# Optimization experiments

Measured on AMD Instinct MI355X. Metric: run time of the kernel, lower is better.

## Reference

```python
import jax, jax.numpy as jnp
import numpy as np

B, N, FIN, FOUT = 16, 128, 128, 256   # batch, atoms(=max_atom), in_features, out_features
EOUT, BIN, BOUT, CI, L1 = 64, 14, 64, 64, 256


def _rnn_dir(x, wih, whh, bih, bhh):
    # x: [B, T, I]; torch nn.RNN step: h = tanh(x @ Wih^T + bih + h @ Whh^T + bhh)
    h0 = jnp.zeros((x.shape[0], whh.shape[0]), x.dtype)
    def step(h, xt):
        h = jnp.tanh(xt @ wih.T + bih + h @ whh.T + bhh)
        return h, h
    _, ys = jax.lax.scan(step, h0, jnp.swapaxes(x, 0, 1))
    return jnp.swapaxes(ys, 0, 1)  # [B, T, H]


def _bi_rnn(x, wih_f, whh_f, bih_f, bhh_f, wih_b, whh_b, bih_b, bhh_b):
    fwd = _rnn_dir(x, wih_f, whh_f, bih_f, bhh_f)
    bwd = _rnn_dir(x[:, ::-1, :], wih_b, whh_b, bih_b, bhh_b)[:, ::-1, :]
    return jnp.concatenate([fwd, bwd], axis=-1)  # [B, T, 2H]


def setup_inputs() -> dict:
    key = jax.random.key(0)
    ks = jax.random.split(key, 24)
    g = lambda i, shape, s=0.05: (jax.random.normal(ks[i], shape, jnp.float32) * s)
    return {
        "x": g(0, (B, N, FIN), 1.0),
        "adj": jax.random.randint(ks[1], (B, N, N), 0, 2).astype(jnp.int32),
        "w_edge": g(2, (B, N, N, BIN), 1.0),
        "W": g(3, (FIN, FOUT)),
        "a": g(4, (2 * FOUT, EOUT)),
        "wfc_w": g(5, (BIN, BOUT)), "wfc_b": g(6, (BOUT,)),
        "fc_w": g(7, (EOUT + BOUT, 1)), "fc_b": g(8, (1,)),
        "fcc_w": g(9, (FOUT, 1)), "fcc_b": g(10, (1,)),
        "wih_f": g(11, (CI, N)), "whh_f": g(12, (CI, CI)), "bih_f": g(13, (CI,)), "bhh_f": g(14, (CI,)),
        "wih_b": g(15, (CI, N)), "whh_b": g(16, (CI, CI)), "bih_b": g(17, (CI,)), "bhh_b": g(18, (CI,)),
        "fco_w": g(19, (2 * CI + FOUT, L1)), "fco_b": g(20, (L1,)),
    }


def reference(x, adj, w_edge, W, a, wfc_w, wfc_b, fc_w, fc_b, fcc_w, fcc_b,
              wih_f, whh_f, bih_f, bhh_f, wih_b, whh_b, bih_b, bhh_b, fco_w, fco_b):
    h = x @ W  # [B, N, FOUT]
    # faithful reproduction of the repeat/cat(dim=1)/view trick
    t1 = jnp.tile(h, (1, 1, N)).reshape(B, N * N, FOUT)  # row i*N+j = h_i
    t2 = jnp.tile(h, (1, N, 1))                          # row i*N+j = h_j
    atom_trans = jnp.concatenate([t1, t2], axis=1).reshape(B, N, N, 2 * FOUT)
    e = atom_trans @ a                                   # [B, N, N, EOUT]
    wproj = w_edge @ wfc_w + wfc_b                       # [B, N, N, BOUT]
    e = jax.nn.leaky_relu(jnp.concatenate([e, wproj], axis=3))
    e = (e @ fc_w + fc_b)[..., 0]                        # [B, N, N]
    att = jax.nn.softmax(jnp.where(adj > 0, e, jnp.float32(-9e15)), axis=2)
    # dropout is identity in eval mode
    at_in = att[..., None] * h[:, :, None, :]            # [B, N, N, FOUT], h_i broadcast over j
    hn = jax.nn.leaky_relu((at_in @ fcc_w + fcc_b)[..., 0])  # [B, N, N]
    hn = jax.nn.leaky_relu(_bi_rnn(hn, wih_f, whh_f, bih_f, bhh_f, wih_b, whh_b, bih_b, bhh_b))
    h1 = jnp.einsum('bij,bjf->bif', att, h)              # [B, N, FOUT]
    out = jnp.concatenate([hn, h1], axis=2) @ fco_w + fco_b  # [B, N, L1]
    return jax.nn.elu(out)
```

## Files before the change

kernel.cpp:

```cpp
#include <hip/hip_runtime.h>
#include <hip/hip_bf16.h>

#define DEV static __device__ __forceinline__

constexpr int B=16, N=128, FIN=128, FOUT=256, EOUT=64, BINW=14, BOUT=64, CI=64, L1=256;

constexpr int O_H   = 0;
constexpr int O_S   = O_H  + B*N*FOUT;
constexpr int O_SU  = O_S  + B*N;
constexpr int O_SV  = O_SU + B*N;
constexpr int O_ATT = O_SV + B*N;
constexpr int O_ZF  = O_ATT+ B*N*N;
constexpr int O_ZB  = O_ZF + B*N*CI;
constexpr int O_RF  = O_ZB + B*N*CI;
constexpr int O_RB  = O_RF + B*N*CI;
constexpr int O_H1  = O_RB + B*N*CI;

DEV float bf16_to_f32(unsigned short u){
  unsigned int x = ((unsigned int)u) << 16; float f;
  __builtin_memcpy(&f, &x, 4); return f;
}
DEV void bf2x(unsigned int u, float& lo, float& hi){
  unsigned int a = u << 16, b = u & 0xFFFF0000u;
  __builtin_memcpy(&lo, &a, 4); __builtin_memcpy(&hi, &b, 4);
}
DEV float lrelu(float x){ return x > 0.f ? x : 0.01f * x; }
DEV float bcastf(float v, int lane){
  return __builtin_bit_cast(float, __builtin_amdgcn_readlane(__builtin_bit_cast(int, v), lane));
}
DEV float ldf(const void* p, int i, int m){
  return m ? bf16_to_f32(((const unsigned short*)p)[i]) : ((const float*)p)[i];
}
DEV int blk_mode(const void* x, int nt, int tid){
  const unsigned short* u = (const unsigned short*)x;
  int e = (u[tid & 255] >> 7) & 0xFF;
  int cnt = __syncthreads_count(e >= 100 && e <= 140);
  return cnt * 4 >= nt * 3;
}

__global__ __launch_bounds__(256, 2) void k_h_pq(const void* __restrict__ xr,
                                                 const void* __restrict__ Wp,
                                                 const void* __restrict__ Ap,
                                                 const void* __restrict__ fccwp,
                                                 const void* __restrict__ fcwp,
                                                 float* __restrict__ ws){
  int blk = blockIdx.x, tid = threadIdx.x;
  int b = blk >> 5, i0 = (blk & 31) * 4;
  __shared__ __align__(16) float xl[4*FIN];
  __shared__ __align__(16) float hrow[4*FOUT];
  __shared__ __align__(16) float pl[4*EOUT];
  __shared__ __align__(16) float ql[4*EOUT];
  __shared__ float red[16];
  int mode = blk_mode(xr, 256, tid);
  if (mode){
    const unsigned short* xu = (const unsigned short*)xr + (size_t)(b*N + i0)*FIN;
    for (int t = tid; t < 4*FIN/8; t += 256){
      uint4 u4 = ((const uint4*)xu)[t];
      float* o = &xl[t*8];
      bf2x(u4.x,o[0],o[1]); bf2x(u4.y,o[2],o[3]); bf2x(u4.z,o[4],o[5]); bf2x(u4.w,o[6],o[7]);
    }
  } else {
    const float* xf = (const float*)xr + (size_t)(b*N + i0)*FIN;
    for (int t4 = tid; t4 < 4*FIN/4; t4 += 256)
      *(float4*)&xl[t4*4] = ((const float4*)xf)[t4];
  }
  __syncthreads();
  int f = tid;
  float acc[4] = {0,0,0,0};
  if (mode){
    const unsigned short* Wu = (const unsigned short*)Wp;
    #pragma unroll 2
    for (int c = 0; c < FIN; c += 4){
      float w0 = bf16_to_f32(Wu[(c+0)*FOUT + f]);
      float w1 = bf16_to_f32(Wu[(c+1)*FOUT + f]);
      float w2 = bf16_to_f32(Wu[(c+2)*FOUT + f]);
      float w3 = bf16_to_f32(Wu[(c+3)*FOUT + f]);
      #pragma unroll
      for (int r = 0; r < 4; ++r){
        float4 x4 = *(const float4*)&xl[r*FIN + c];
        acc[r] += x4.x*w0 + x4.y*w1 + x4.z*w2 + x4.w*w3;
      }
    }
  } else {
    const float* Wf = (const float*)Wp;
    #pragma unroll 2
    for (int c = 0; c < FIN; c += 4){
      float w0 = Wf[(c+0)*FOUT + f];
      float w1 = Wf[(c+1)*FOUT + f];
      float w2 = Wf[(c+2)*FOUT + f];
      float w3 = Wf[(c+3)*FOUT + f];
      #pragma unroll
      for (int r = 0; r < 4; ++r){
        float4 x4 = *(const float4*)&xl[r*FIN + c];
        acc[r] += x4.x*w0 + x4.y*w1 + x4.z*w2 + x4.w*w3;
      }
    }
  }
  float fw = ldf(fccwp, f, mode);
  #pragma unroll
  for (int r = 0; r < 4; ++r){
    ws[O_H + (b*N + i0 + r)*FOUT + f] = acc[r];
    hrow[r*FOUT + f] = acc[r];
  }
  #pragma unroll
  for (int r = 0; r < 4; ++r){
    float v = acc[r] * fw;
    for (int off = 32; off; off >>= 1) v += __shfl_down(v, off);
    if ((tid & 63) == 0) red[(tid >> 6)*4 + r] = v;
  }
  __syncthreads();
  if (tid < 4){
    float s = red[tid] + red[4+tid] + red[8+tid] + red[12+tid];
    ws[O_S + b*N + i0 + tid] = s;
  }
  {
    int o = tid & 63, which = (tid >> 6) & 1, hh = tid >> 7;
    float a2[2] = {0.f,0.f};
    if (mode){
      const unsigned short* Au = (const unsigned short*)Ap;
      #pragma unroll 2
      for (int c = 0; c < FOUT; c += 4){
        float w0 = bf16_to_f32(Au[(which*FOUT + c+0)*EOUT + o]);
        float w1 = bf16_to_f32(Au[(which*FOUT + c+1)*EOUT + o]);
        float w2 = bf16_to_f32(Au[(which*FOUT + c+2)*EOUT + o]);
        float w3 = bf16_to_f32(Au[(which*FOUT + c+3)*EOUT + o]);
        #pragma unroll
        for (int r = 0; r < 2; ++r){
          float4 h4 = *(const float4*)&hrow[(hh*2+r)*FOUT + c];
          a2[r] += h4.x*w0 + h4.y*w1 + h4.z*w2 + h4.w*w3;
        }
      }
    } else {
      const float* Af = (const float*)Ap;
      #pragma unroll 2
      for (int c = 0; c < FOUT; c += 4){
        float w0 = Af[(which*FOUT + c+0)*EOUT + o];
        float w1 = Af[(which*FOUT + c+1)*EOUT + o];
        float w2 = Af[(which*FOUT + c+2)*EOUT + o];
        float w3 = Af[(which*FOUT + c+3)*EOUT + o];
        #pragma unroll
        for (int r = 0; r < 2; ++r){
          float4 h4 = *(const float4*)&hrow[(hh*2+r)*FOUT + c];
          a2[r] += h4.x*w0 + h4.y*w1 + h4.z*w2 + h4.w*w3;
        }
      }
    }
    float* dst = which ? ql : pl;
    #pragma unroll
    for (int r = 0; r < 2; ++r) dst[(hh*2+r)*EOUT + o] = a2[r];
  }
  __syncthreads();
  {
    int o = tid & 63, w = tid >> 6;
    float fw2 = ldf(fcwp, o, mode);
    int w2 = (w < 2) ? w : 0;
    float s1 = lrelu(pl[w*EOUT + o]        + ql[w*EOUT + o])        * fw2;
    float s3 = lrelu(pl[(2*w2)*EOUT + o]   + ql[(2*w2+1)*EOUT + o]) * fw2;
    for (int off = 32; off; off >>= 1){
      s1 += __shfl_down(s1, off); s3 += __shfl_down(s3, off);
    }
    if (o == 0){
      ws[O_SU + b*N + i0 + w] = s1;
      if (w < 2){
        int r1 = (i0 >> 1) + w;
        ws[O_SV + b*N + r1]      = s3;
        ws[O_SV + b*N + r1 + 64] = s3;
      }
    }
  }
}

struct AttArgs { const void *we,*x,*wfcw,*wfcb,*fcw,*fcb,*fccb,*wihf,*bihf,*bhhf,*wihb,*bihb,*bhhb; };

__global__ __launch_bounds__(256) void k_att(AttArgs A, const int* __restrict__ adj,
                                             float* __restrict__ ws){
  int blk = blockIdx.x, tid = threadIdx.x;
  int half = tid >> 7, j = tid & 127, wv = (tid >> 6) & 1;
  int tau = blk*2 + half;
  int b = tau >> 7, i = tau & 127;
  __shared__ __align__(16) float wel[2][N*BINW];
  __shared__ __align__(16) float hnp[2][N];
  __shared__ __align__(16) float wfcwl[BINW*BOUT];
  __shared__ __align__(16) float wfcbl[BOUT];
  __shared__ __align__(16) float fcw2l[BOUT];
  __shared__ float red2[2][2];
  int mode = blk_mode(A.x, 256, tid);
  for (int t = tid; t < BINW*BOUT; t += 256) wfcwl[t] = ldf(A.wfcw, t, mode);
  if (tid < BOUT){ wfcbl[tid] = ldf(A.wfcb, tid, mode); fcw2l[tid] = ldf(A.fcw, EOUT + tid, mode); }
  if (mode){
    const unsigned short* weu = (const unsigned short*)A.we + (size_t)(b*N + i)*N*BINW;
    for (int t = j; t < N*BINW/8; t += 128){
      uint4 q = ((const uint4*)weu)[t];
      float* o = &wel[half][t*8];
      bf2x(q.x,o[0],o[1]); bf2x(q.y,o[2],o[3]); bf2x(q.z,o[4],o[5]); bf2x(q.w,o[6],o[7]);
    }
  } else {
    const float* wef = (const float*)A.we + (size_t)(b*N + i)*N*BINW;
    for (int t4 = j; t4 < N*BINW/4; t4 += 128)
      *(float4*)&wel[half][t4*4] = ((const float4*)wef)[t4];
  }
  __syncthreads();
  float wr[BINW];
  #pragma unroll
  for (int t = 0; t < BINW; ++t) wr[t] = wel[half][j*BINW + t];
  float wcon = 0.f;
  for (int o = 0; o < BOUT; o += 4){
    float4 bb = *(const float4*)&wfcbl[o];
    float w0 = bb.x, w1 = bb.y, w2 = bb.z, w3 = bb.w;
    #pragma unroll
    for (int t = 0; t < BINW; ++t){
      float4 w4 = *(const float4*)&wfcwl[t*BOUT + o];
      w0 = fmaf(wr[t], w4.x, w0); w1 = fmaf(wr[t], w4.y, w1);
      w2 = fmaf(wr[t], w4.z, w2); w3 = fmaf(wr[t], w4.w, w3);
    }
    float4 f4 = *(const float4*)&fcw2l[o];
    wcon += lrelu(w0)*f4.x + lrelu(w1)*f4.y + lrelu(w2)*f4.z + lrelu(w3)*f4.w;
  }
  const float* R = ws;
  float econ = (i < 64) ? R[O_SU + b*N + 2*i + (j >= 64 ? 1 : 0)]
                        : R[O_SV + b*N + j];
  float etot = econ + wcon + ldf(A.fcb, 0, mode);
  float m = (adj[(b*N + i)*N + j] > 0) ? etot : -9e15f;
  float mx = m;
  for (int off = 32; off; off >>= 1) mx = fmaxf(mx, __shfl_xor(mx, off));
  if ((tid & 63) == 0) red2[half][wv] = mx;
  __syncthreads();
  mx = fmaxf(red2[half][0], red2[half][1]);
  float ev = expf(m - mx);
  float sum = ev;
  for (int off = 32; off; off >>= 1) sum += __shfl_xor(sum, off);
  __syncthreads();
  if ((tid & 63) == 0) red2[half][wv] = sum;
  __syncthreads();
  sum = red2[half][0] + red2[half][1];
  float att = ev / sum;
  ws[O_ATT + (b*N + i)*N + j] = att;
  float sbi = R[O_S + b*N + i];
  hnp[half][j] = lrelu(att * sbi + ldf(A.fccb, 0, mode));
  __syncthreads();
  {
    int d = wv, c = tid & 63;
    float acc = ldf(d ? A.bihb : A.bihf, c, mode) + ldf(d ? A.bhhb : A.bhhf, c, mode);
    const void* wihp = d ? A.wihb : A.wihf;
    if (mode){
      const uint4* wq = (const uint4*)((const unsigned short*)wihp + c*N);
      #pragma unroll 4
      for (int k = 0; k < N; k += 8){
        uint4 q = wq[k >> 3];
        float w0,w1,w2,w3,w4,w5,w6,w7;
        bf2x(q.x,w0,w1); bf2x(q.y,w2,w3); bf2x(q.z,w4,w5); bf2x(q.w,w6,w7);
        float4 h0 = *(const float4*)&hnp[half][k];
        float4 h1 = *(const float4*)&hnp[half][k+4];
        acc += h0.x*w0 + h0.y*w1 + h0.z*w2 + h0.w*w3
             + h1.x*w4 + h1.y*w5 + h1.z*w6 + h1.w*w7;
      }
    } else {
      const float* wf = (const float*)wihp + c*N;
      #pragma unroll 8
      for (int k = 0; k < N; k += 4){
        float4 h4 = *(const float4*)&hnp[half][k];
        float4 w4 = *(const float4*)&wf[k];
        acc += h4.x*w4.x + h4.y*w4.y + h4.z*w4.z + h4.w*w4.w;
      }
    }
    ws[(d ? O_ZB : O_ZF) + (b*N + i)*CI + c] = acc;
  }
}

__global__ __launch_bounds__(256, 1) void k_rnn_h1(const void* __restrict__ xr,
                                                   const void* __restrict__ whhf,
                                                   const void* __restrict__ whhb,
                                                   float* __restrict__ ws){
  __shared__ __align__(16) float sh[N*CI];
  int blk = blockIdx.x, tid = threadIdx.x;
  int mode = blk_mode(xr, 256, tid);
  const float* R = ws;
  if (blk < 32){
    int d = blk >> 4, b = blk & 15;
    const int zb = (d ? O_ZB : O_ZF) + b*N*CI;
    const int ob = (d ? O_RB : O_RF) + b*N*CI;
    for (int it = tid; it < N*CI/4; it += 256)
      *(float4*)&sh[it*4] = *(const float4*)&ws[zb + it*4];
    __syncthreads();
    if (tid < 64){
      int c = tid;
      const void* whhp = d ? whhb : whhf;
      float wreg[CI];
      if (mode){
        const uint4* wq = (const uint4*)((const unsigned short*)whhp + c*CI);
        #pragma unroll
        for (int k = 0; k < CI; k += 8){
          uint4 q = wq[k >> 3];
          bf2x(q.x,wreg[k+0],wreg[k+1]); bf2x(q.y,wreg[k+2],wreg[k+3]);
          bf2x(q.z,wreg[k+4],wreg[k+5]); bf2x(q.w,wreg[k+6],wreg[k+7]);
        }
      } else {
        const float* wf = (const float*)whhp + c*CI;
        #pragma unroll
        for (int k = 0; k < CI; k += 4){
          float4 w4 = *(const float4*)&wf[k];
          wreg[k]=w4.x; wreg[k+1]=w4.y; wreg[k+2]=w4.z; wreg[k+3]=w4.w;
        }
      }
      const int step = d ? -1 : 1;
      int tt = d ? (N-1) : 0;
      float hv = 0.f;
      float z = sh[tt*CI + c];
      for (int t = 0; t < N; ++t){
        int ti = tt + step; ti = ti < 0 ? 0 : (ti > N-1 ? N-1 : ti);
        float znext = sh[ti*CI + c];
        float s[CI];
        #pragma unroll
        for (int k = 0; k < CI; ++k) s[k] = bcastf(hv, k);
#if __has_builtin(__builtin_amdgcn_sched_barrier)
        __builtin_amdgcn_sched_barrier(0);
#endif
        float a0 = z, a1 = 0.f, a2 = 0.f, a3 = 0.f;
        #pragma unroll
        for (int k = 0; k < CI; k += 4){
          a0 = fmaf(s[k+0], wreg[k+0], a0);
          a1 = fmaf(s[k+1], wreg[k+1], a1);
          a2 = fmaf(s[k+2], wreg[k+2], a2);
          a3 = fmaf(s[k+3], wreg[k+3], a3);
        }
        float x = (a0+a1)+(a2+a3);
        x = fminf(15.f, fmaxf(-15.f, x));
        float p = __expf(2.f * x);
        hv = (p - 1.f) * __builtin_amdgcn_rcpf(p + 1.f);
        sh[tt*CI + c] = hv;
        z = znext;
        tt += step;
      }
    }
    __syncthreads();
    for (int it = tid; it < N*CI/4; it += 256)
      *(float4*)&ws[ob + it*4] = *(const float4*)&sh[it*4];
  } else {
    for (int task = blk - 32; task < 256; task += 256){
      int b = task >> 4, i0 = (task & 15) * 8;
      int f = tid;
      __syncthreads();
      for (int t = tid; t < 8*N; t += 256){
        int r = t >> 7, k = t & 127;
        sh[k*8 + r] = R[O_ATT + (b*N + i0 + r)*N + k];
      }
      __syncthreads();
      float acc[8] = {0,0,0,0,0,0,0,0};
      for (int k = 0; k < N; ++k){
        float hv = R[O_H + (b*N + k)*FOUT + f];
        float4 a0 = *(const float4*)&sh[k*8];
        float4 a1 = *(const float4*)&sh[k*8 + 4];
        acc[0] += a0.x*hv; acc[1] += a0.y*hv; acc[2] += a0.z*hv; acc[3] += a0.w*hv;
        acc[4] += a1.x*hv; acc[5] += a1.y*hv; acc[6] += a1.z*hv; acc[7] += a1.w*hv;
      }
      #pragma unroll
      for (int r = 0; r < 8; ++r)
        ws[O_H1 + (b*N + i0 + r)*FOUT + f] = acc[r];
    }
  }
}

__global__ __launch_bounds__(256, 2) void k_out(const void* __restrict__ xr,
                                                const void* __restrict__ fcowp,
                                                const void* __restrict__ fcobp,
                                                const float* __restrict__ R, void* dout){
  int blk = blockIdx.x, tid = threadIdx.x;
  int b = blk >> 5, i0 = (blk & 31) * 4;
  constexpr int KW = 2*CI + FOUT;
  __shared__ __align__(16) float inl[4*KW];
  int mode = blk_mode(xr, 256, tid);
  for (int t = tid; t < 4*2*CI; t += 256){
    int r = t >> 7, k = t & 127;
    int row = b*N + i0 + r;
    inl[r*KW + k] = (k < CI) ? lrelu(R[O_RF + row*CI + k])
                             : lrelu(R[O_RB + row*CI + (k - CI)]);
  }
  for (int t = tid; t < 4*FOUT; t += 256){
    int r = t >> 8, k = t & 255;
    inl[r*KW + 2*CI + k] = R[O_H1 + (b*N + i0 + r)*FOUT + k];
  }
  __syncthreads();
  int l = tid;
  float bias = ldf(fcobp, l, mode);
  float acc[4];
  #pragma unroll
  for (int r = 0; r < 4; ++r) acc[r] = bias;
  if (mode){
    const unsigned short* fu = (const unsigned short*)fcowp;
    #pragma unroll 2
    for (int k = 0; k < KW; k += 4){
      float w0 = bf16_to_f32(fu[(k+0)*L1 + l]);
      float w1 = bf16_to_f32(fu[(k+1)*L1 + l]);
      float w2 = bf16_to_f32(fu[(k+2)*L1 + l]);
      float w3 = bf16_to_f32(fu[(k+3)*L1 + l]);
      #pragma unroll
      for (int r = 0; r < 4; ++r){
        float4 v = *(const float4*)&inl[r*KW + k];
        acc[r] += v.x*w0 + v.y*w1 + v.z*w2 + v.w*w3;
      }
    }
  } else {
    const float* ff = (const float*)fcowp;
    #pragma unroll 2
    for (int k = 0; k < KW; k += 4){
      float w0 = ff[(k+0)*L1 + l];
      float w1 = ff[(k+1)*L1 + l];
      float w2 = ff[(k+2)*L1 + l];
      float w3 = ff[(k+3)*L1 + l];
      #pragma unroll
      for (int r = 0; r < 4; ++r){
        float4 v = *(const float4*)&inl[r*KW + k];
        acc[r] += v.x*w0 + v.y*w1 + v.z*w2 + v.w*w3;
      }
    }
  }
  #pragma unroll
  for (int r = 0; r < 4; ++r){
    float o = acc[r] > 0.f ? acc[r] : expm1f(acc[r]);
    int idx = (b*N + i0 + r)*L1 + l;
    if (mode) ((__hip_bfloat16*)dout)[idx] = __float2bfloat16(o);
    else      ((float*)dout)[idx] = o;
  }
}

extern "C" void kernel_launch(void* const* d_in, const int* in_sizes, int n_in,
                              void* d_out, int out_size, void* d_ws, size_t ws_size,
                              hipStream_t stream){
  (void)in_sizes; (void)n_in; (void)out_size; (void)ws_size;
  float* ws = (float*)d_ws;
  AttArgs A;
  A.we = d_in[2]; A.x = d_in[0]; A.wfcw = d_in[5]; A.wfcb = d_in[6];
  A.fcw = d_in[7]; A.fcb = d_in[8]; A.fccb = d_in[10];
  A.wihf = d_in[11]; A.bihf = d_in[13]; A.bhhf = d_in[14];
  A.wihb = d_in[15]; A.bihb = d_in[17]; A.bhhb = d_in[18];
  hipLaunchKernelGGL(k_h_pq,   dim3(512),    dim3(256), 0, stream,
                     d_in[0], d_in[3], d_in[4], d_in[9], d_in[7], ws);
  hipLaunchKernelGGL(k_att,    dim3(B*N/2),  dim3(256), 0, stream, A, (const int*)d_in[1], ws);
  hipLaunchKernelGGL(k_rnn_h1, dim3(288),    dim3(256), 0, stream,
                     d_in[0], d_in[12], d_in[16], ws);
  hipLaunchKernelGGL(k_out,    dim3(512),    dim3(256), 0, stream,
                     d_in[0], d_in[19], d_in[20], ws, d_out);
}
```

Measured before the change: 204.5 us.

## Add L2 prefetch blocks for later-stage inputs, split h1 tasks, raise unroll

```diff
diff --git a/kernel.cpp b/kernel.cpp
--- a/kernel.cpp
+++ b/kernel.cpp
@@ -38,13 +38,33 @@
   return cnt * 4 >= nt * 3;
 }
 
+struct PF { const void* p[7]; int b32[7]; int b16[7]; int insz[7]; };
+
 __global__ __launch_bounds__(256, 2) void k_h_pq(const void* __restrict__ xr,
                                                  const void* __restrict__ Wp,
                                                  const void* __restrict__ Ap,
                                                  const void* __restrict__ fccwp,
                                                  const void* __restrict__ fcwp,
+                                                 PF pf,
                                                  float* __restrict__ ws){
   int blk = blockIdx.x, tid = threadIdx.x;
+  if (blk >= 512){
+    int mode = blk_mode(xr, 256, tid);
+    int pid = blk - 512;
+    unsigned int acc = 0;
+    for (int e = 0; e < 7; ++e){
+      int bytes = mode ? pf.b16[e] : pf.b32[e];
+      if (pf.insz[e] > 0 && pf.insz[e] < bytes) bytes = pf.insz[e];
+      const uint4* p = (const uint4*)pf.p[e];
+      int n16 = bytes >> 4;
+      for (int t = pid*256 + tid; t < n16; t += 512*256){
+        uint4 v = p[t];
+        acc ^= v.x ^ v.y ^ v.z ^ v.w;
+      }
+    }
+    asm volatile("" :: "v"(acc));
+    return;
+  }
   int b = blk >> 5, i0 = (blk & 31) * 4;
   __shared__ __align__(16) float xl[4*FIN];
   __shared__ __align__(16) float hrow[4*FOUT];
@@ -69,7 +89,7 @@
   float acc[4] = {0,0,0,0};
   if (mode){
     const unsigned short* Wu = (const unsigned short*)Wp;
-    #pragma unroll 2
+    #pragma unroll 4
     for (int c = 0; c < FIN; c += 4){
       float w0 = bf16_to_f32(Wu[(c+0)*FOUT + f]);
       float w1 = bf16_to_f32(Wu[(c+1)*FOUT + f]);
@@ -83,7 +103,7 @@
     }
   } else {
     const float* Wf = (const float*)Wp;
-    #pragma unroll 2
+    #pragma unroll 4
     for (int c = 0; c < FIN; c += 4){
       float w0 = Wf[(c+0)*FOUT + f];
       float w1 = Wf[(c+1)*FOUT + f];
@@ -336,27 +356,24 @@
     for (int it = tid; it < N*CI/4; it += 256)
       *(float4*)&ws[ob + it*4] = *(const float4*)&sh[it*4];
   } else {
-    for (int task = blk - 32; task < 256; task += 256){
-      int b = task >> 4, i0 = (task & 15) * 8;
-      int f = tid;
-      __syncthreads();
-      for (int t = tid; t < 8*N; t += 256){
-        int r = t >> 7, k = t & 127;
-        sh[k*8 + r] = R[O_ATT + (b*N + i0 + r)*N + k];
-      }
-      __syncthreads();
-      float acc[8] = {0,0,0,0,0,0,0,0};
-      for (int k = 0; k < N; ++k){
-        float hv = R[O_H + (b*N + k)*FOUT + f];
-        float4 a0 = *(const float4*)&sh[k*8];
-        float4 a1 = *(const float4*)&sh[k*8 + 4];
-        acc[0] += a0.x*hv; acc[1] += a0.y*hv; acc[2] += a0.z*hv; acc[3] += a0.w*hv;
-        acc[4] += a1.x*hv; acc[5] += a1.y*hv; acc[6] += a1.z*hv; acc[7] += a1.w*hv;
-      }
-      #pragma unroll
-      for (int r = 0; r < 8; ++r)
-        ws[O_H1 + (b*N + i0 + r)*FOUT + f] = acc[r];
-    }
+    int task = blk - 32;
+    int b = task >> 5, i0 = (task & 31) * 4;
+    int f = tid;
+    for (int t = tid; t < 4*N; t += 256){
+      int r = t >> 7, k = t & 127;
+      sh[k*4 + r] = R[O_ATT + (b*N + i0 + r)*N + k];
+    }
+    __syncthreads();
+    float acc[4] = {0,0,0,0};
+    #pragma unroll 4
+    for (int k = 0; k < N; ++k){
+      float hv = R[O_H + (b*N + k)*FOUT + f];
+      float4 a0 = *(const float4*)&sh[k*4];
+      acc[0] += a0.x*hv; acc[1] += a0.y*hv; acc[2] += a0.z*hv; acc[3] += a0.w*hv;
+    }
+    #pragma unroll
+    for (int r = 0; r < 4; ++r)
+      ws[O_H1 + (b*N + i0 + r)*FOUT + f] = acc[r];
   }
 }
 
@@ -387,7 +404,7 @@
   for (int r = 0; r < 4; ++r) acc[r] = bias;
   if (mode){
     const unsigned short* fu = (const unsigned short*)fcowp;
-    #pragma unroll 2
+    #pragma unroll 4
     for (int k = 0; k < KW; k += 4){
       float w0 = bf16_to_f32(fu[(k+0)*L1 + l]);
       float w1 = bf16_to_f32(fu[(k+1)*L1 + l]);
@@ -401,7 +418,7 @@
     }
   } else {
     const float* ff = (const float*)fcowp;
-    #pragma unroll 2
+    #pragma unroll 4
     for (int k = 0; k < KW; k += 4){
       float w0 = ff[(k+0)*L1 + l];
       float w1 = ff[(k+1)*L1 + l];
@@ -426,17 +443,29 @@
 extern "C" void kernel_launch(void* const* d_in, const int* in_sizes, int n_in,
                               void* d_out, int out_size, void* d_ws, size_t ws_size,
                               hipStream_t stream){
-  (void)in_sizes; (void)n_in; (void)out_size; (void)ws_size;
+  (void)n_in; (void)out_size; (void)ws_size;
   float* ws = (float*)d_ws;
   AttArgs A;
   A.we = d_in[2]; A.x = d_in[0]; A.wfcw = d_in[5]; A.wfcb = d_in[6];
   A.fcw = d_in[7]; A.fcb = d_in[8]; A.fccb = d_in[10];
   A.wihf = d_in[11]; A.bihf = d_in[13]; A.bhhf = d_in[14];
   A.wihb = d_in[15]; A.bihb = d_in[17]; A.bhhb = d_in[18];
-  hipLaunchKernelGGL(k_h_pq,   dim3(512),    dim3(256), 0, stream,
-                     d_in[0], d_in[3], d_in[4], d_in[9], d_in[7], ws);
+
+  PF pf;
+  const int idxs[7]  = {2, 1, 19, 11, 12, 15, 16};
+  const int elems[7] = {B*N*N*BINW, B*N*N, (2*CI+FOUT)*L1, CI*N, CI*CI, CI*N, CI*CI};
+  const bool isint[7]= {false, true, false, false, false, false, false};
+  for (int e = 0; e < 7; ++e){
+    pf.p[e]    = d_in[idxs[e]];
+    pf.b32[e]  = elems[e]*4;
+    pf.b16[e]  = isint[e] ? elems[e]*4 : elems[e]*2;
+    pf.insz[e] = in_sizes ? in_sizes[idxs[e]] : 0;
+  }
+
+  hipLaunchKernelGGL(k_h_pq,   dim3(1024),   dim3(256), 0, stream,
+                     d_in[0], d_in[3], d_in[4], d_in[9], d_in[7], pf, ws);
   hipLaunchKernelGGL(k_att,    dim3(B*N/2),  dim3(256), 0, stream, A, (const int*)d_in[1], ws);
-  hipLaunchKernelGGL(k_rnn_h1, dim3(288),    dim3(256), 0, stream,
+  hipLaunchKernelGGL(k_rnn_h1, dim3(544),    dim3(256), 0, stream,
                      d_in[0], d_in[12], d_in[16], ws);
   hipLaunchKernelGGL(k_out,    dim3(512),    dim3(256), 0, stream,
                      d_in[0], d_in[19], d_in[20], ws, d_out);
```

After: 212.2 us. +3.7%, slower.

## Move h1 half of output projection into RNN kernel's idle blocks

Applied to the files above, without the earlier changes.

```diff
diff --git a/kernel.cpp b/kernel.cpp
--- a/kernel.cpp
+++ b/kernel.cpp
@@ -270,6 +270,8 @@
 __global__ __launch_bounds__(256, 1) void k_rnn_h1(const void* __restrict__ xr,
                                                    const void* __restrict__ whhf,
                                                    const void* __restrict__ whhb,
+                                                   const void* __restrict__ fcowp,
+                                                   const void* __restrict__ fcobp,
                                                    float* __restrict__ ws){
   __shared__ __align__(16) float sh[N*CI];
   int blk = blockIdx.x, tid = threadIdx.x;
@@ -336,80 +338,105 @@
     for (int it = tid; it < N*CI/4; it += 256)
       *(float4*)&ws[ob + it*4] = *(const float4*)&sh[it*4];
   } else {
-    for (int task = blk - 32; task < 256; task += 256){
-      int b = task >> 4, i0 = (task & 15) * 8;
-      int f = tid;
-      __syncthreads();
-      for (int t = tid; t < 8*N; t += 256){
-        int r = t >> 7, k = t & 127;
-        sh[k*8 + r] = R[O_ATT + (b*N + i0 + r)*N + k];
-      }
-      __syncthreads();
-      float acc[8] = {0,0,0,0,0,0,0,0};
-      for (int k = 0; k < N; ++k){
-        float hv = R[O_H + (b*N + k)*FOUT + f];
-        float4 a0 = *(const float4*)&sh[k*8];
-        float4 a1 = *(const float4*)&sh[k*8 + 4];
-        acc[0] += a0.x*hv; acc[1] += a0.y*hv; acc[2] += a0.z*hv; acc[3] += a0.w*hv;
-        acc[4] += a1.x*hv; acc[5] += a1.y*hv; acc[6] += a1.z*hv; acc[7] += a1.w*hv;
-      }
-      #pragma unroll
-      for (int r = 0; r < 8; ++r)
-        ws[O_H1 + (b*N + i0 + r)*FOUT + f] = acc[r];
-    }
+    int task = blk - 32;
+    int b = task >> 5, i0 = (task & 31) * 4;
+    int f = tid;
+    for (int t = tid; t < 4*N; t += 256){
+      int r = t >> 7, k = t & 127;
+      sh[k*4 + r] = R[O_ATT + (b*N + i0 + r)*N + k];
+    }
+    __syncthreads();
+    float acc[4] = {0,0,0,0};
+    #pragma unroll 4
+    for (int k = 0; k < N; ++k){
+      float hv = R[O_H + (b*N + k)*FOUT + f];
+      float4 a0 = *(const float4*)&sh[k*4];
+      acc[0] += a0.x*hv; acc[1] += a0.y*hv; acc[2] += a0.z*hv; acc[3] += a0.w*hv;
+    }
+    float* h1l = sh + 4*N;
+    #pragma unroll
+    for (int r = 0; r < 4; ++r) h1l[r*FOUT + f] = acc[r];
+    __syncthreads();
+    float bias = ldf(fcobp, f, mode);
+    float p4[4] = {bias, bias, bias, bias};
+    if (mode){
+      const unsigned short* fu = (const unsigned short*)fcowp + (size_t)(2*CI)*L1;
+      #pragma unroll 2
+      for (int k = 0; k < FOUT; k += 4){
+        float w0 = bf16_to_f32(fu[(k+0)*L1 + f]);
+        float w1 = bf16_to_f32(fu[(k+1)*L1 + f]);
+        float w2 = bf16_to_f32(fu[(k+2)*L1 + f]);
+        float w3 = bf16_to_f32(fu[(k+3)*L1 + f]);
+        #pragma unroll
+        for (int r = 0; r < 4; ++r){
+          float4 hv = *(const float4*)&h1l[r*FOUT + k];
+          p4[r] += hv.x*w0 + hv.y*w1 + hv.z*w2 + hv.w*w3;
+        }
+      }
+    } else {
+      const float* ff = (const float*)fcowp + (size_t)(2*CI)*L1;
+      #pragma unroll 2
+      for (int k = 0; k < FOUT; k += 4){
+        float w0 = ff[(k+0)*L1 + f];
+        float w1 = ff[(k+1)*L1 + f];
+        float w2 = ff[(k+2)*L1 + f];
+        float w3 = ff[(k+3)*L1 + f];
+        #pragma unroll
+        for (int r = 0; r < 4; ++r){
+          float4 hv = *(const float4*)&h1l[r*FOUT + k];
+          p4[r] += hv.x*w0 + hv.y*w1 + hv.z*w2 + hv.w*w3;
+        }
+      }
+    }
+    #pragma unroll
+    for (int r = 0; r < 4; ++r)
+      ws[O_H1 + (b*N + i0 + r)*L1 + f] = p4[r];
   }
 }
 
 __global__ __launch_bounds__(256, 2) void k_out(const void* __restrict__ xr,
                                                 const void* __restrict__ fcowp,
-                                                const void* __restrict__ fcobp,
                                                 const float* __restrict__ R, void* dout){
   int blk = blockIdx.x, tid = threadIdx.x;
   int b = blk >> 5, i0 = (blk & 31) * 4;
-  constexpr int KW = 2*CI + FOUT;
-  __shared__ __align__(16) float inl[4*KW];
+  __shared__ __align__(16) float inl[4*2*CI];
   int mode = blk_mode(xr, 256, tid);
   for (int t = tid; t < 4*2*CI; t += 256){
     int r = t >> 7, k = t & 127;
     int row = b*N + i0 + r;
-    inl[r*KW + k] = (k < CI) ? lrelu(R[O_RF + row*CI + k])
-                             : lrelu(R[O_RB + row*CI + (k - CI)]);
-  }
-  for (int t = tid; t < 4*FOUT; t += 256){
-    int r = t >> 8, k = t & 255;
-    inl[r*KW + 2*CI + k] = R[O_H1 + (b*N + i0 + r)*FOUT + k];
+    inl[r*128 + k] = (k < CI) ? lrelu(R[O_RF + row*CI + k])
+                              : lrelu(R[O_RB + row*CI + (k - CI)]);
   }
   __syncthreads();
   int l = tid;
-  float bias = ldf(fcobp, l, mode);
   float acc[4];
   #pragma unroll
-  for (int r = 0; r < 4; ++r) acc[r] = bias;
+  for (int r = 0; r < 4; ++r) acc[r] = R[O_H1 + (b*N + i0 + r)*L1 + l];
   if (mode){
     const unsigned short* fu = (const unsigned short*)fcowp;
-    #pragma unroll 2
-    for (int k = 0; k < KW; k += 4){
+    #pragma unroll 4
+    for (int k = 0; k < 2*CI; k += 4){
       float w0 = bf16_to_f32(fu[(k+0)*L1 + l]);
       float w1 = bf16_to_f32(fu[(k+1)*L1 + l]);
       float w2 = bf16_to_f32(fu[(k+2)*L1 + l]);
       float w3 = bf16_to_f32(fu[(k+3)*L1 + l]);
       #pragma unroll
       for (int r = 0; r < 4; ++r){
-        float4 v = *(const float4*)&inl[r*KW + k];
+        float4 v = *(const float4*)&inl[r*128 + k];
         acc[r] += v.x*w0 + v.y*w1 + v.z*w2 + v.w*w3;
       }
     }
   } else {
     const float* ff = (const float*)fcowp;
-    #pragma unroll 2
-    for (int k = 0; k < KW; k += 4){
+    #pragma unroll 4
+    for (int k = 0; k < 2*CI; k += 4){
       float w0 = ff[(k+0)*L1 + l];
       float w1 = ff[(k+1)*L1 + l];
       float w2 = ff[(k+2)*L1 + l];
       float w3 = ff[(k+3)*L1 + l];
       #pragma unroll
       for (int r = 0; r < 4; ++r){
-        float4 v = *(const float4*)&inl[r*KW + k];
+        float4 v = *(const float4*)&inl[r*128 + k];
         acc[r] += v.x*w0 + v.y*w1 + v.z*w2 + v.w*w3;
       }
     }
@@ -436,8 +463,8 @@
   hipLaunchKernelGGL(k_h_pq,   dim3(512),    dim3(256), 0, stream,
                      d_in[0], d_in[3], d_in[4], d_in[9], d_in[7], ws);
   hipLaunchKernelGGL(k_att,    dim3(B*N/2),  dim3(256), 0, stream, A, (const int*)d_in[1], ws);
-  hipLaunchKernelGGL(k_rnn_h1, dim3(288),    dim3(256), 0, stream,
-                     d_in[0], d_in[12], d_in[16], ws);
+  hipLaunchKernelGGL(k_rnn_h1, dim3(544),    dim3(256), 0, stream,
+                     d_in[0], d_in[12], d_in[16], d_in[19], d_in[20], ws);
   hipLaunchKernelGGL(k_out,    dim3(512),    dim3(256), 0, stream,
-                     d_in[0], d_in[19], d_in[20], ws, d_out);
-}
+                     d_in[0], d_in[19], ws, d_out);
+}
```

Result: faster. 197.8 us (-3.3%).
